# Kernel tuning notes

Hardware: AMD Instinct MI355X
Metric: run time of the kernel (lower is better)

The kernel has to match this reference:

```python
import jax, jax.numpy as jnp
import numpy as np
import math

HIDDEN = 768
KEY = 128      # attention_key_size
INTER = 1536   # intermediate_size
B, S = 4, 2048


def setup_inputs() -> dict:
    key = jax.random.key(0)
    ks = jax.random.split(key, 8)
    hidden_states = jax.random.normal(ks[0], (B, S, HIDDEN), dtype=jnp.float32)
    attention_mask = jax.random.randint(ks[1], (B, 1, 1, S), 0, 2, dtype=jnp.int32)
    position_ids = jnp.arange(B * S, dtype=jnp.int32).reshape(B, S) % S
    Wi = jax.random.normal(ks[2], (HIDDEN, 2 * INTER + KEY), dtype=jnp.float32) * 0.02
    bi = jnp.zeros((2 * INTER + KEY,), dtype=jnp.float32)
    gamma = jax.random.normal(ks[3], (2, KEY), dtype=jnp.float32) * 0.02 + 1.0
    beta = jnp.zeros((2, KEY), dtype=jnp.float32)
    Wo = jax.random.normal(ks[4], (INTER, HIDDEN), dtype=jnp.float32) * 0.02
    bo = jnp.zeros((HIDDEN,), dtype=jnp.float32)
    return {"hidden_states": hidden_states, "attention_mask": attention_mask,
            "position_ids": position_ids, "Wi": Wi, "bi": bi,
            "gamma": gamma, "beta": beta, "Wo": Wo, "bo": bo}


def _gau_forward(hidden_states, attention_mask, Wi, bi, gamma, beta, Wo, bo):
    # i_dense + swish activation
    h = jax.nn.silu(jnp.einsum('bsd,de->bse', hidden_states, Wi) + bi)
    u = h[..., :INTER]
    v = h[..., INTER:2 * INTER]
    qk = h[..., 2 * INTER:]
    # OffsetScale: per-head affine (heads=2 -> q, k)
    q = qk * gamma[0] + beta[0]
    k = qk * gamma[1] + beta[1]
    scores = jnp.einsum('bid,bjd->bij', q, k) / math.sqrt(KEY)
    # additive mask: (1 - m) * -1e12, squeeze head dim
    am = (1.0 - attention_mask.astype(scores.dtype)) * -1e12
    scores = scores + am[:, 0]  # [B,1,S] broadcasts over query dim
    # softmax_plus normalization: scale logits by log(l)/log(512)
    valid = (scores > -1e11).astype(scores.dtype)
    l = jnp.maximum(jnp.sum(valid, axis=-1, keepdims=True), 1.0)
    scale = jnp.log(l) / jnp.log(jnp.asarray(512.0, scores.dtype))
    attn = jax.nn.softmax(scores * scale, axis=-1)
    ctx = jnp.einsum('bij,bjd->bid', attn, v)
    return jnp.einsum('bse,eh->bsh', u * ctx, Wo) + bo


def reference(hidden_states, attention_mask, position_ids, Wi, bi, gamma, beta, Wo, bo):
    # position_ids unused: p_bias is not 'rotary'
    return _gau_forward(hidden_states, attention_mask, Wi, bi, gamma, beta, Wo, bo)
```

## Files before the change

kernel.cpp:

```cpp
#include <hip/hip_runtime.h>
#include <math.h>

#define HIDDEN 768
#define KEY    128
#define INTER  1536
#define NB     4
#define SEQ    2048
#define MTOT   (NB*SEQ)
#define ETOT   (2*INTER+KEY)
#define CS     136

typedef short bf16x8 __attribute__((ext_vector_type(8)));
typedef float f32x4  __attribute__((ext_vector_type(4)));
typedef unsigned short u16x8 __attribute__((ext_vector_type(8)));

__device__ __forceinline__ unsigned short f2bfbits(float x) {
    union { float f; unsigned int u; } a; a.f = x;
    unsigned int r = a.u + 0x7fffu + ((a.u >> 16) & 1u);
    return (unsigned short)(r >> 16);
}
__device__ __forceinline__ float bfbits2f(unsigned short b) {
    union { float f; unsigned int u; } a; a.u = ((unsigned int)b) << 16;
    return a.f;
}

__device__ __forceinline__ void gl2lds16(const unsigned short* g, unsigned short* l) {
    __builtin_amdgcn_global_load_lds(
        (const __attribute__((address_space(1))) unsigned int*)g,
        (__attribute__((address_space(3))) unsigned int*)l, 16, 0, 0);
}

__device__ __forceinline__ void transpose_tile(
    const float* __restrict__ in, unsigned short* __restrict__ out,
    int R, int C, int c0, int r0, int tid, unsigned short tile[32][33])
{
    int tx = tid & 31, ty4 = (tid >> 5)*4;
    #pragma unroll
    for (int rr = 0; rr < 4; rr++) {
        int r = ty4 + rr;
        tile[r][tx] = f2bfbits(in[(size_t)(r0+r)*C + c0+tx]);
    }
    __syncthreads();
    #pragma unroll
    for (int rr = 0; rr < 4; rr++) {
        int r = ty4 + rr;
        out[(size_t)(c0+r)*R + r0+tx] = tile[tx][r];
    }
}

__global__ __launch_bounds__(256) void prep_kernel(
    const float* __restrict__ X, const float* __restrict__ Wi,
    const float* __restrict__ Wo, const int* __restrict__ mask,
    unsigned short* __restrict__ Xb, unsigned short* __restrict__ WiT,
    unsigned short* __restrict__ WoT, float* __restrict__ scaleb)
{
    __shared__ unsigned short tile[32][33];
    __shared__ int red[256];
    const int bid = blockIdx.x, tid = threadIdx.x;
    if (bid < 3072) {
        int i = bid*256 + tid;
        const float4* in4 = (const float4*)X;
        float4 a = in4[(size_t)i*2], b = in4[(size_t)i*2+1];
        u16x8 o;
        o[0]=f2bfbits(a.x); o[1]=f2bfbits(a.y); o[2]=f2bfbits(a.z); o[3]=f2bfbits(a.w);
        o[4]=f2bfbits(b.x); o[5]=f2bfbits(b.y); o[6]=f2bfbits(b.z); o[7]=f2bfbits(b.w);
        *(u16x8*)&Xb[(size_t)i*8] = o;
    } else if (bid < 5472) {
        int t = bid - 3072;
        transpose_tile(Wi, WiT, HIDDEN, ETOT, (t%100)*32, (t/100)*32, tid, tile);
    } else if (bid < 6624) {
        int t = bid - 5472;
        transpose_tile(Wo, WoT, INTER, HIDDEN, (t%24)*32, (t/24)*32, tid, tile);
    } else {
        int b = bid - 6624;
        int s = 0;
        for (int j = tid; j < SEQ; j += 256)
            s += (mask[b*SEQ + j] != 0) ? 1 : 0;
        red[tid] = s;
        __syncthreads();
        for (int step = 128; step > 0; step >>= 1) {
            if (tid < step) red[tid] += red[tid + step];
            __syncthreads();
        }
        if (tid == 0) {
            float l = fmaxf((float)red[0], 1.0f);
            scaleb[b] = logf(l) / logf(512.0f);
        }
    }
}

template<int BK>
__device__ __forceinline__ void mfma_core(
    const unsigned short* __restrict__ Abase, int lda,
    const unsigned short* __restrict__ Bbase, int ldb,
    unsigned short* As, unsigned short* Bs,
    f32x4 acc[4][4], int tid, int ktot)
{
    const int lane = tid & 63, wave = tid >> 6;
    const int wm = (wave >> 1) << 6, wn = (wave & 1) << 6;
    const int lm = lane & 15;
    const int q8 = (lane >> 4) << 3;
    const int row_a = tid >> 2, col_a = (tid & 3) << 3;
    const int row_b = row_a + 64;

    for (int k0 = 0; k0 < ktot; k0 += BK) {
        if (k0) __syncthreads();
        #pragma unroll
        for (int h = 0; h < BK/32; h++) {
            gl2lds16(Abase + (size_t)row_a*lda + k0 + h*32 + col_a, As + h*4096 + tid*8);
            gl2lds16(Abase + (size_t)row_b*lda + k0 + h*32 + col_a, As + h*4096 + (tid+256)*8);
            gl2lds16(Bbase + (size_t)row_a*ldb + k0 + h*32 + col_a, Bs + h*4096 + tid*8);
            gl2lds16(Bbase + (size_t)row_b*ldb + k0 + h*32 + col_a, Bs + h*4096 + (tid+256)*8);
        }
        __syncthreads();
        #pragma unroll
        for (int h = 0; h < BK/32; h++) {
            const unsigned short* Ah = As + h*4096;
            const unsigned short* Bh = Bs + h*4096;
            bf16x8 af[4], bfr[4];
            #pragma unroll
            for (int i = 0; i < 4; i++)
                af[i] = *(const bf16x8*)&Ah[(wm + i*16 + lm)*32 + q8];
            #pragma unroll
            for (int j = 0; j < 4; j++)
                bfr[j] = *(const bf16x8*)&Bh[(wn + j*16 + lm)*32 + q8];
            #pragma unroll
            for (int i = 0; i < 4; i++)
                #pragma unroll
                for (int j = 0; j < 4; j++)
                    acc[i][j] = __builtin_amdgcn_mfma_f32_16x16x32_bf16(af[i], bfr[j], acc[i][j], 0, 0, 0);
        }
    }
}

#define EPILOG_IDX \
    const int lane = tid & 63, wave = tid >> 6; \
    const int wm = (wave >> 1) << 6, wn = (wave & 1) << 6; \
    const int cn = lane & 15, r4 = (lane >> 4) << 2;

__global__ __launch_bounds__(256, 4) void gemm1_mfma(
    const unsigned short* __restrict__ Xb, const unsigned short* __restrict__ WiT,
    const float* __restrict__ bi, const float* __restrict__ gamma, const float* __restrict__ beta,
    unsigned short* __restrict__ u, unsigned short* __restrict__ vT,
    unsigned short* __restrict__ qb, unsigned short* __restrict__ kb)
{
    __shared__ __align__(16) unsigned short smem[128*CS];
    unsigned short* As = smem;
    unsigned short* Bs = smem + 4096;
    const int tid = threadIdx.x;
    const int bid = blockIdx.x;
    const int xcd = bid & 7, slot = bid >> 3;
    const int xt = slot >> 3;
    const int yt = (xcd << 3) + (slot & 7);
    const int row0 = yt*128, col0 = xt*128;
    f32x4 acc[4][4];
    #pragma unroll
    for (int i = 0; i < 4; i++)
        #pragma unroll
        for (int j = 0; j < 4; j++)
            acc[i][j] = (f32x4){0.f,0.f,0.f,0.f};
    mfma_core<32>(Xb + (size_t)row0*HIDDEN, HIDDEN, WiT + (size_t)col0*HIDDEN, HIDDEN,
                  As, Bs, acc, tid, HIDDEN);
    EPILOG_IDX
    __syncthreads();
    #pragma unroll
    for (int j = 0; j < 4; j++) {
        int nl = wn + j*16 + cn;
        float bin = bi[col0 + nl];
        #pragma unroll
        for (int i = 0; i < 4; i++) {
            #pragma unroll
            for (int r = 0; r < 4; r++) {
                int rowl = wm + i*16 + r4 + r;
                float x = acc[i][j][r] + bin;
                float h = x / (1.0f + __expf(-x));
                smem[rowl*CS + nl] = f2bfbits(h);
            }
        }
    }
    __syncthreads();
    if (col0 < INTER) {
        #pragma unroll
        for (int rnd = 0; rnd < 8; rnd++) {
            int row = rnd*16 + (tid>>4);
            int col = (tid&15)*8;
            u16x8 h = *(const u16x8*)&smem[row*CS + col];
            *(u16x8*)&u[(size_t)(row0+row)*INTER + col0 + col] = h;
        }
    } else if (col0 < 2*INTER) {
        int c = tid >> 1;
        int half = tid & 1;
        int b = row0 / SEQ;
        int srow = row0 - b*SEQ + half*64;
        size_t base = ((size_t)b*INTER + (col0 - INTER) + c)*SEQ + srow;
        #pragma unroll
        for (int k = 0; k < 8; k++) {
            u16x8 h;
            #pragma unroll
            for (int t = 0; t < 8; t++)
                h[t] = smem[(half*64 + k*8 + t)*CS + c];
            *(u16x8*)&vT[base + k*8] = h;
        }
    } else {
        #pragma unroll
        for (int rnd = 0; rnd < 8; rnd++) {
            int row = rnd*16 + (tid>>4);
            int col = (tid&15)*8;
            u16x8 h = *(const u16x8*)&smem[row*CS + col];
            int m = row0 + row;
            u16x8 qo, ko;
            #pragma unroll
            for (int t = 0; t < 8; t++) {
                float hv = bfbits2f(h[t]);
                qo[t] = f2bfbits(hv*gamma[col+t]     + beta[col+t]);
                ko[t] = f2bfbits(hv*gamma[KEY+col+t] + beta[KEY+col+t]);
            }
            *(u16x8*)&qb[(size_t)m*KEY + col] = qo;
            *(u16x8*)&kb[(size_t)m*KEY + col] = ko;
        }
    }
}

__global__ __launch_bounds__(256, 4) void attn_mfma(
    const unsigned short* __restrict__ qb, const unsigned short* __restrict__ kb,
    const int* __restrict__ mask, const float* __restrict__ scaleb,
    unsigned short* __restrict__ P, float* __restrict__ lpart)
{
    __shared__ __align__(16) unsigned short smem[128*CS];
    unsigned short* As = smem;
    unsigned short* Bs = smem + 8192;
    const int tid = threadIdx.x;
    const int z = blockIdx.z;
    const int row0 = blockIdx.y*128, col0 = blockIdx.x*128;
    f32x4 acc[4][4];
    #pragma unroll
    for (int i = 0; i < 4; i++)
        #pragma unroll
        for (int j = 0; j < 4; j++)
            acc[i][j] = (f32x4){0.f,0.f,0.f,0.f};
    mfma_core<64>(qb + ((size_t)z*SEQ + row0)*KEY, KEY, kb + ((size_t)z*SEQ + col0)*KEY, KEY,
                  As, Bs, acc, tid, KEY);
    const float st = scaleb[z] * 0.08838834764831845f;
    EPILOG_IDX
    __syncthreads();
    #pragma unroll
    for (int j = 0; j < 4; j++) {
        int nl = wn + j*16 + cn;
        float mkf = (mask[z*SEQ + col0 + nl] != 0) ? 1.0f : 0.0f;
        #pragma unroll
        for (int i = 0; i < 4; i++) {
            #pragma unroll
            for (int r = 0; r < 4; r++) {
                int rowl = wm + i*16 + r4 + r;
                float p = mkf * __expf(acc[i][j][r]*st);
                smem[rowl*CS + nl] = f2bfbits(p);
            }
        }
    }
    __syncthreads();
    #pragma unroll
    for (int rnd = 0; rnd < 8; rnd++) {
        int row = rnd*16 + (tid>>4);
        int col = (tid&15)*8;
        u16x8 h = *(const u16x8*)&smem[row*CS + col];
        *(u16x8*)&P[((size_t)z*SEQ + row0 + row)*SEQ + col0 + col] = h;
        float s8 = 0.f;
        #pragma unroll
        for (int t = 0; t < 8; t++) s8 += bfbits2f(h[t]);
        #pragma unroll
        for (int off = 8; off > 0; off >>= 1) s8 += __shfl_xor(s8, off, 16);
        if ((tid & 15) == 0)
            lpart[(size_t)blockIdx.x*MTOT + (size_t)z*SEQ + row0 + row] = s8;
    }
}

__global__ __launch_bounds__(256, 4) void pv_mfma(
    const unsigned short* __restrict__ P, const unsigned short* __restrict__ vT,
    const float* __restrict__ lpart, unsigned short* __restrict__ u)
{
    __shared__ __align__(16) unsigned short smem[128*CS];
    __shared__ float ls[128];
    unsigned short* As = smem;
    unsigned short* Bs = smem + 8192;
    const int tid = threadIdx.x;
    const int bid = blockIdx.x;
    const int xcd = bid & 7, slot = bid >> 3;
    const int z = slot / 24, pos = slot % 24;
    const int yt = (xcd & 3)*4 + pos/6;
    const int xt = (xcd >> 2)*6 + pos%6;
    const int row0 = yt*128, col0 = xt*128;
    if (tid < 128) {
        float s = 0.f;
        #pragma unroll
        for (int t = 0; t < 16; t++)
            s += lpart[(size_t)t*MTOT + (size_t)z*SEQ + row0 + tid];
        ls[tid] = s;
    }
    f32x4 acc[4][4];
    #pragma unroll
    for (int i = 0; i < 4; i++)
        #pragma unroll
        for (int j = 0; j < 4; j++)
            acc[i][j] = (f32x4){0.f,0.f,0.f,0.f};
    mfma_core<64>(P + ((size_t)z*SEQ + row0)*SEQ, SEQ, vT + ((size_t)z*INTER + col0)*SEQ, SEQ,
                  As, Bs, acc, tid, SEQ);
    EPILOG_IDX
    __syncthreads();
    #pragma unroll
    for (int j = 0; j < 4; j++) {
        int nl = wn + j*16 + cn;
        #pragma unroll
        for (int i = 0; i < 4; i++) {
            #pragma unroll
            for (int r = 0; r < 4; r++) {
                int rowl = wm + i*16 + r4 + r;
                smem[rowl*CS + nl] = f2bfbits(acc[i][j][r]);
            }
        }
    }
    __syncthreads();
    #pragma unroll
    for (int rnd = 0; rnd < 8; rnd++) {
        int row = rnd*16 + (tid>>4);
        int col = (tid&15)*8;
        int m = z*SEQ + row0 + row;
        float linv = 1.0f / ls[row];
        u16x8 cx = *(const u16x8*)&smem[row*CS + col];
        size_t idx = (size_t)m*INTER + col0 + col;
        u16x8 uu = *(const u16x8*)&u[idx];
        u16x8 g;
        #pragma unroll
        for (int t = 0; t < 8; t++)
            g[t] = f2bfbits(bfbits2f(uu[t]) * bfbits2f(cx[t]) * linv);
        *(u16x8*)&u[idx] = g;
    }
}

__global__ __launch_bounds__(256, 4) void gemm2_mfma(
    const unsigned short* __restrict__ g, const unsigned short* __restrict__ WoT,
    const float* __restrict__ bo, float* __restrict__ out)
{
    __shared__ __align__(16) unsigned short As[8192];
    __shared__ __align__(16) unsigned short Bs[4096];
    const int tid = threadIdx.x;
    const int bid = blockIdx.x;
    const int xcd = bid & 7, slot = bid >> 3;
    const int xt = slot >> 3;
    const int yt = (xcd << 3) + (slot & 7);
    const int row0 = yt*128, col0 = xt*64;
    const int lane = tid & 63, wave = tid >> 6;
    const int wm = (wave >> 1) << 6;
    const int wn = (wave & 1) << 5;
    const int lm = lane & 15;
    const int q8 = (lane >> 4) << 3;
    const int row_a = tid >> 2, col_a = (tid & 3) << 3;
    f32x4 acc[4][2];
    #pragma unroll
    for (int i = 0; i < 4; i++)
        #pragma unroll
        for (int j = 0; j < 2; j++)
            acc[i][j] = (f32x4){0.f,0.f,0.f,0.f};
    const unsigned short* Abase = g + (size_t)row0*INTER;
    const unsigned short* Bbase = WoT + (size_t)col0*INTER;
    for (int k0 = 0; k0 < INTER; k0 += 64) {
        if (k0) __syncthreads();
        #pragma unroll
        for (int h = 0; h < 2; h++) {
            gl2lds16(Abase + (size_t)row_a*INTER + k0 + h*32 + col_a,      As + h*4096 + tid*8);
            gl2lds16(Abase + (size_t)(row_a+64)*INTER + k0 + h*32 + col_a, As + h*4096 + (tid+256)*8);
            gl2lds16(Bbase + (size_t)row_a*INTER + k0 + h*32 + col_a,      Bs + h*2048 + tid*8);
        }
        __syncthreads();
        #pragma unroll
        for (int h = 0; h < 2; h++) {
            const unsigned short* Ah = As + h*4096;
            const unsigned short* Bh = Bs + h*2048;
            bf16x8 af[4], bfr[2];
            #pragma unroll
            for (int i = 0; i < 4; i++)
                af[i] = *(const bf16x8*)&Ah[(wm + i*16 + lm)*32 + q8];
            #pragma unroll
            for (int j = 0; j < 2; j++)
                bfr[j] = *(const bf16x8*)&Bh[(wn + j*16 + lm)*32 + q8];
            #pragma unroll
            for (int i = 0; i < 4; i++)
                #pragma unroll
                for (int j = 0; j < 2; j++)
                    acc[i][j] = __builtin_amdgcn_mfma_f32_16x16x32_bf16(af[i], bfr[j], acc[i][j], 0, 0, 0);
        }
    }
    const int cn = lane & 15, r4 = (lane >> 4) << 2;
    #pragma unroll
    for (int j = 0; j < 2; j++) {
        int n = col0 + wn + j*16 + cn;
        float bon = bo[n];
        #pragma unroll
        for (int i = 0; i < 4; i++) {
            #pragma unroll
            for (int r = 0; r < 4; r++) {
                int m = row0 + wm + i*16 + r4 + r;
                out[(size_t)m*HIDDEN + n] = acc[i][j][r] + bon;
            }
        }
    }
}

extern "C" void kernel_launch(void* const* d_in, const int* in_sizes, int n_in,
                              void* d_out, int out_size, void* d_ws, size_t ws_size,
                              hipStream_t stream)
{
    const float* X     = (const float*)d_in[0];
    const int*   mask  = (const int*)d_in[1];
    const float* Wi    = (const float*)d_in[3];
    const float* bi    = (const float*)d_in[4];
    const float* gamma = (const float*)d_in[5];
    const float* beta  = (const float*)d_in[6];
    const float* Wo    = (const float*)d_in[7];
    const float* bo    = (const float*)d_in[8];
    float* out = (float*)d_out;

    unsigned short* Xb  = (unsigned short*)d_ws;
    unsigned short* WiT = Xb  + (size_t)MTOT*HIDDEN;
    unsigned short* WoT = WiT + (size_t)ETOT*HIDDEN;
    unsigned short* u   = WoT + (size_t)HIDDEN*INTER;
    unsigned short* vT  = u   + (size_t)MTOT*INTER;
    unsigned short* qb  = vT  + (size_t)MTOT*INTER;
    unsigned short* kb  = qb  + (size_t)MTOT*KEY;
    unsigned short* P   = kb  + (size_t)MTOT*KEY;
    float* scb   = (float*)(P + (size_t)NB*SEQ*SEQ);
    float* lpart = scb + 8;

    prep_kernel<<<6628, 256, 0, stream>>>(X, Wi, Wo, mask, Xb, WiT, WoT, scb);
    gemm1_mfma<<<1600, 256, 0, stream>>>(Xb, WiT, bi, gamma, beta, u, vT, qb, kb);
    attn_mfma<<<dim3(SEQ/128, SEQ/128, NB), 256, 0, stream>>>(qb, kb, mask, scb, P, lpart);
    pv_mfma<<<768, 256, 0, stream>>>(P, vT, lpart, u);
    gemm2_mfma<<<768, 256, 0, stream>>>(u, WoT, bo, out);
}
```

Before: 267.1 us.

## Halve PV kernel tile height to 64 rows and double grid for occupancy

The P·V kernel now uses 64x128 output tiles instead of 128x128, launching twice as many blocks with a custom inline K-loop in place of the shared mfma_core. Each wave computes a 64x32 slice with fewer accumulators, and launch bounds rise to 6 blocks per CU. The intent is better CU fill and latency hiding for the 768-block grid. In exchange, reuse of the vT tile drops, so vT is read from global memory twice as often.

Measured after the change: 283.4 us. 6.1% more time.

```diff
diff --git a/kernel.cpp b/kernel.cpp
--- a/kernel.cpp
+++ b/kernel.cpp
@@ -274,53 +274,84 @@
     }
 }
 
-__global__ __launch_bounds__(256, 4) void pv_mfma(
+__global__ __launch_bounds__(256, 6) void pv_mfma(
     const unsigned short* __restrict__ P, const unsigned short* __restrict__ vT,
     const float* __restrict__ lpart, unsigned short* __restrict__ u)
 {
-    __shared__ __align__(16) unsigned short smem[128*CS];
-    __shared__ float ls[128];
+    __shared__ __align__(16) unsigned short smem[12288];
+    __shared__ float ls[64];
     unsigned short* As = smem;
-    unsigned short* Bs = smem + 8192;
+    unsigned short* Bs = smem + 4096;
     const int tid = threadIdx.x;
     const int bid = blockIdx.x;
     const int xcd = bid & 7, slot = bid >> 3;
-    const int z = slot / 24, pos = slot % 24;
-    const int yt = (xcd & 3)*4 + pos/6;
+    const int z = slot / 48, pos = slot % 48;
+    const int yt = (xcd & 3)*8 + pos/6;
     const int xt = (xcd >> 2)*6 + pos%6;
-    const int row0 = yt*128, col0 = xt*128;
-    if (tid < 128) {
+    const int row0 = yt*64, col0 = xt*128;
+    if (tid < 64) {
         float s = 0.f;
         #pragma unroll
         for (int t = 0; t < 16; t++)
             s += lpart[(size_t)t*MTOT + (size_t)z*SEQ + row0 + tid];
         ls[tid] = s;
     }
-    f32x4 acc[4][4];
+    const int lane = tid & 63, wave = tid >> 6;
+    const int wn = wave << 5;
+    const int lm = lane & 15, q8 = (lane >> 4) << 3;
+    const int row_a = tid >> 2, col_a = (tid & 3) << 3;
+    const unsigned short* Abase = P + ((size_t)z*SEQ + row0)*SEQ;
+    const unsigned short* Bbase = vT + ((size_t)z*INTER + col0)*SEQ;
+    f32x4 acc[4][2];
     #pragma unroll
     for (int i = 0; i < 4; i++)
         #pragma unroll
-        for (int j = 0; j < 4; j++)
+        for (int j = 0; j < 2; j++)
             acc[i][j] = (f32x4){0.f,0.f,0.f,0.f};
-    mfma_core<64>(P + ((size_t)z*SEQ + row0)*SEQ, SEQ, vT + ((size_t)z*INTER + col0)*SEQ, SEQ,
-                  As, Bs, acc, tid, SEQ);
-    EPILOG_IDX
-    __syncthreads();
-    #pragma unroll
-    for (int j = 0; j < 4; j++) {
+    for (int k0 = 0; k0 < SEQ; k0 += 64) {
+        if (k0) __syncthreads();
+        #pragma unroll
+        for (int h = 0; h < 2; h++) {
+            gl2lds16(Abase + (size_t)row_a*SEQ + k0 + h*32 + col_a,      As + h*2048 + tid*8);
+            gl2lds16(Bbase + (size_t)row_a*SEQ + k0 + h*32 + col_a,      Bs + h*4096 + tid*8);
+            gl2lds16(Bbase + (size_t)(row_a+64)*SEQ + k0 + h*32 + col_a, Bs + h*4096 + 2048 + tid*8);
+        }
+        __syncthreads();
+        #pragma unroll
+        for (int h = 0; h < 2; h++) {
+            const unsigned short* Ah = As + h*2048;
+            const unsigned short* Bh = Bs + h*4096;
+            bf16x8 af[4], bfr[2];
+            #pragma unroll
+            for (int i = 0; i < 4; i++)
+                af[i] = *(const bf16x8*)&Ah[(i*16 + lm)*32 + q8];
+            #pragma unroll
+            for (int j = 0; j < 2; j++)
+                bfr[j] = *(const bf16x8*)&Bh[(wn + j*16 + lm)*32 + q8];
+            #pragma unroll
+            for (int i = 0; i < 4; i++)
+                #pragma unroll
+                for (int j = 0; j < 2; j++)
+                    acc[i][j] = __builtin_amdgcn_mfma_f32_16x16x32_bf16(af[i], bfr[j], acc[i][j], 0, 0, 0);
+        }
+    }
+    const int cn = lane & 15, r4 = (lane >> 4) << 2;
+    __syncthreads();
+    #pragma unroll
+    for (int j = 0; j < 2; j++) {
         int nl = wn + j*16 + cn;
         #pragma unroll
         for (int i = 0; i < 4; i++) {
             #pragma unroll
             for (int r = 0; r < 4; r++) {
-                int rowl = wm + i*16 + r4 + r;
+                int rowl = i*16 + r4 + r;
                 smem[rowl*CS + nl] = f2bfbits(acc[i][j][r]);
             }
         }
     }
     __syncthreads();
     #pragma unroll
-    for (int rnd = 0; rnd < 8; rnd++) {
+    for (int rnd = 0; rnd < 4; rnd++) {
         int row = rnd*16 + (tid>>4);
         int col = (tid&15)*8;
         int m = z*SEQ + row0 + row;
@@ -433,6 +464,6 @@
     prep_kernel<<<6628, 256, 0, stream>>>(X, Wi, Wo, mask, Xb, WiT, WoT, scb);
     gemm1_mfma<<<1600, 256, 0, stream>>>(Xb, WiT, bi, gamma, beta, u, vT, qb, kb);
     attn_mfma<<<dim3(SEQ/128, SEQ/128, NB), 256, 0, stream>>>(qb, kb, mask, scb, P, lpart);
-    pv_mfma<<<768, 256, 0, stream>>>(P, vT, lpart, u);
+    pv_mfma<<<1536, 256, 0, stream>>>(P, vT, lpart, u);
     gemm2_mfma<<<768, 256, 0, stream>>>(u, WoT, bo, out);
 }
```
